# Optimization experiments

Hardware: AMD Instinct MI355X
Metric: run time of the kernel (lower is better)

The kernel has to match this reference:

```python
import jax, jax.numpy as jnp
import numpy as np

D_MODEL = 384
HEADS = 8
DIM_HEAD = D_MODEL // HEADS
IH = IW = 32
N = IH * IW
D_FF = 1536
EPS = 1e-5


def _relative_index():
    # replicates torch buffer construction (meshgrid 'ij')
    gy, gx = np.meshgrid(np.arange(IH), np.arange(IW), indexing='ij')
    coords = np.stack([gy, gx]).reshape(2, -1)              # [2, N]
    rel = coords[:, :, None] - coords[:, None, :]           # [2, N, N]
    rel[0] += IH - 1
    rel[1] += IW - 1
    rel[0] *= 2 * IW - 1
    return (rel[0] + rel[1]).reshape(-1)                    # [N*N] int


def setup_inputs() -> dict:
    key = jax.random.key(0)
    ks = jax.random.split(key, 16)
    s = 0.02
    return {
        'src': jax.random.normal(ks[0], (8, N, D_MODEL), jnp.float32),
        'pos': jax.random.normal(ks[1], (8, N, D_MODEL), jnp.float32),
        'rel_bias_table': jax.random.normal(ks[2], ((2 * IH - 1) * (2 * IW - 1), HEADS), jnp.float32) * s,
        'Wq': jax.random.normal(ks[3], (D_MODEL, D_MODEL), jnp.float32) * s,
        'Wk': jax.random.normal(ks[4], (D_MODEL, D_MODEL), jnp.float32) * s,
        'Wv': jax.random.normal(ks[5], (D_MODEL, D_MODEL), jnp.float32) * s,
        'Wo': jax.random.normal(ks[6], (D_MODEL, D_MODEL), jnp.float32) * s,
        'bo': jnp.zeros((D_MODEL,), jnp.float32),
        'W1': jax.random.normal(ks[7], (D_MODEL, D_FF), jnp.float32) * s,
        'b1': jnp.zeros((D_FF,), jnp.float32),
        'W2': jax.random.normal(ks[8], (D_FF, D_MODEL), jnp.float32) * s,
        'b2': jnp.zeros((D_MODEL,), jnp.float32),
        'g1': jnp.ones((D_MODEL,), jnp.float32),
        'be1': jnp.zeros((D_MODEL,), jnp.float32),
        'g2': jnp.ones((D_MODEL,), jnp.float32),
        'be2': jnp.zeros((D_MODEL,), jnp.float32),
    }


def _layernorm(x, g, b):
    mu = jnp.mean(x, -1, keepdims=True)
    var = jnp.var(x, -1, keepdims=True)
    return (x - mu) * jax.lax.rsqrt(var + EPS) * g + b


def _heads(x):
    b, n, _ = x.shape
    return x.reshape(b, n, HEADS, DIM_HEAD).transpose(0, 2, 1, 3)  # [b,h,n,d]


def reference(src, pos, rel_bias_table, Wq, Wk, Wv, Wo, bo, W1, b1, W2, b2, g1, be1, g2, be2):
    rel_idx = _relative_index()
    qk_in = src + pos
    q = _heads(qk_in @ Wq)
    k = _heads(qk_in @ Wk)
    v = _heads(src @ Wv)
    # relative bias: [heads, n, n]
    bias = rel_bias_table[rel_idx].reshape(N, N, HEADS).transpose(2, 0, 1)
    # relative_bias_x = (x^T @ bias)^T  ==  sum_m bias[h,m,n] * x[b,h,m,d]
    q = q + jnp.einsum('hmn,bhmd->bhnd', bias, q)
    k = k + jnp.einsum('hmn,bhmd->bhnd', bias, k)
    v = v + jnp.einsum('hmn,bhmd->bhnd', bias, v)
    scale = DIM_HEAD ** -0.5
    dots = jnp.einsum('bhnd,bhmd->bhnm', q, k) * scale
    attn = jax.nn.softmax(dots, axis=-1)
    out = jnp.einsum('bhnm,bhmd->bhnd', attn, v)
    out = out.transpose(0, 2, 1, 3).reshape(src.shape[0], N, D_MODEL)
    out = out @ Wo + bo
    x = _layernorm(src + out, g1, be1)
    ff = jax.nn.gelu(x @ W1 + b1, approximate=False) @ W2 + b2
    return _layernorm(x + ff, g2, be2)
```

## Files before the change

kernel.cpp:

```cpp
#include <hip/hip_runtime.h>
#include <math.h>

#define D_MODEL 384
#define HEADS 8
#define DIM_HEAD 48
#define NTOK 1024
#define BATCH 8
#define D_FF 1536
#define LN_EPS 1e-5f

typedef unsigned short u16;
typedef unsigned int u32;
typedef unsigned long long u64;
typedef short short8 __attribute__((ext_vector_type(8)));
typedef float f32x4 __attribute__((ext_vector_type(4)));

union F8 { short8 v; u64 q[2]; u16 u[8]; uint4 u4; };

__device__ __forceinline__ u16 f2bf(float f) {
    union { float f; unsigned u; } c; c.f = f;
    unsigned r = c.u + 0x7FFFu + ((c.u >> 16) & 1u);
    return (u16)(r >> 16);
}
__device__ __forceinline__ float bf2f(u16 u) {
    union { unsigned u; float f; } c; c.u = ((unsigned)u) << 16; return c.f;
}
__device__ __forceinline__ void gload_lds16(const u16* g, u16* l) {
    __builtin_amdgcn_global_load_lds(
        (const __attribute__((address_space(1))) void*)g,
        (__attribute__((address_space(3))) void*)l, 16, 0, 0);
}

__global__ __launch_bounds__(256) void add_cast_kernel(
        const float4* __restrict__ a, const float4* __restrict__ b,
        ushort4* __restrict__ o1, ushort4* __restrict__ o2, int n4) {
    int i = blockIdx.x * blockDim.x + threadIdx.x;
    if (i >= n4) return;
    float4 x = a[i], y = b[i];
    ushort4 u1, u2;
    u1.x = f2bf(x.x + y.x); u1.y = f2bf(x.y + y.y); u1.z = f2bf(x.z + y.z); u1.w = f2bf(x.w + y.w);
    u2.x = f2bf(x.x); u2.y = f2bf(x.y); u2.z = f2bf(x.z); u2.w = f2bf(x.w);
    o1[i] = u1; o2[i] = u2;
}

__global__ __launch_bounds__(256) void castT4_kernel(
        const float* __restrict__ i0, const float* __restrict__ i1,
        const float* __restrict__ i2, const float* __restrict__ i3,
        u16* __restrict__ o0, u16* __restrict__ o1,
        u16* __restrict__ o2, u16* __restrict__ o3) {
    const float* in  = (blockIdx.z == 0) ? i0 : (blockIdx.z == 1) ? i1 : (blockIdx.z == 2) ? i2 : i3;
    u16*         out = (blockIdx.z == 0) ? o0 : (blockIdx.z == 1) ? o1 : (blockIdx.z == 2) ? o2 : o3;
    __shared__ float t[32][33];
    int c0 = blockIdx.x * 32, r0 = blockIdx.y * 32;
    int tx = threadIdx.x, ty = threadIdx.y;
    for (int i = ty; i < 32; i += 8)
        t[i][tx] = in[(long)(r0 + i) * 384 + c0 + tx];
    __syncthreads();
    for (int i = ty; i < 32; i += 8)
        out[(long)(c0 + i) * 384 + r0 + tx] = f2bf(t[tx][i]);
}

__global__ __launch_bounds__(256) void castT_kernel(
        const float* __restrict__ in, u16* __restrict__ out, int R, int C) {
    __shared__ float t[32][33];
    int c0 = blockIdx.x * 32, r0 = blockIdx.y * 32;
    int tx = threadIdx.x, ty = threadIdx.y;
    for (int i = ty; i < 32; i += 8)
        t[i][tx] = in[(long)(r0 + i) * C + c0 + tx];
    __syncthreads();
    for (int i = ty; i < 32; i += 8)
        out[(long)(c0 + i) * R + r0 + tx] = f2bf(t[tx][i]);
}

__global__ __launch_bounds__(256) void biasT_bf16_kernel(const float* __restrict__ table,
                                                         u16* __restrict__ BT) {
    long i = (long)blockIdx.x * blockDim.x + threadIdx.x;
    const long total = (long)HEADS * NTOK * NTOK;
    if (i >= total) return;
    int m = (int)(i & 1023);
    int n = (int)((i >> 10) & 1023);
    int h = (int)(i >> 20);
    int dy = (m >> 5) - (n >> 5) + 31;
    int dx = (m & 31) - (n & 31) + 31;
    BT[i] = f2bf(table[(dy * 63 + dx) * HEADS + h]);
}

template<int OUTMODE, bool HAS_BIAS, bool HAS_RES, bool GELU_>
__global__ __launch_bounds__(256) void mgemm128_kernel(
        const u16* __restrict__ Ab, const u16* __restrict__ Btb,
        float* __restrict__ Cf, u16* __restrict__ Cb, u16* __restrict__ Ct,
        const float* __restrict__ bias, const float* __restrict__ Rb,
        int Kd, int lda, int ldbt, int ldc, int ldr) {
    __shared__ u16 As[2][128 * 32];
    __shared__ u16 Bs[2][128 * 32];
    int tid = threadIdx.x, wave = tid >> 6, lane = tid & 63, g = lane >> 4, l15 = lane & 15;
    int wm = wave >> 1, wn = wave & 1;
    int row0 = blockIdx.y * 128, col0 = blockIdx.x * 128;

    f32x4 acc[4][4] = {};

    int sr = lane >> 2, sk = lane & 3;
    const u16* aG0 = Ab  + (long)(row0 + wave * 16 + sr) * lda  + sk * 8;
    const u16* aG1 = Ab  + (long)(row0 + (wave + 4) * 16 + sr) * lda  + sk * 8;
    const u16* bG0 = Btb + (long)(col0 + wave * 16 + sr) * ldbt + sk * 8;
    const u16* bG1 = Btb + (long)(col0 + (wave + 4) * 16 + sr) * ldbt + sk * 8;
    int w0off = (wave * 16) * 32, w1off = ((wave + 4) * 16) * 32;

    const int T = Kd >> 5;
    gload_lds16(aG0, &As[0][w0off]);
    gload_lds16(aG1, &As[0][w1off]);
    gload_lds16(bG0, &Bs[0][w0off]);
    gload_lds16(bG1, &Bs[0][w1off]);
    __builtin_amdgcn_sched_barrier(0);

    for (int t = 0; t < T; ++t) {
        int cur = t & 1, nxt = cur ^ 1;
        if (t + 1 < T) {
            int k1 = (t + 1) << 5;
            gload_lds16(aG0 + k1, &As[nxt][w0off]);
            gload_lds16(aG1 + k1, &As[nxt][w1off]);
            gload_lds16(bG0 + k1, &Bs[nxt][w0off]);
            gload_lds16(bG1 + k1, &Bs[nxt][w1off]);
            __builtin_amdgcn_sched_barrier(0);
            asm volatile("s_waitcnt vmcnt(4)" ::: "memory");
        } else {
            asm volatile("s_waitcnt vmcnt(0)" ::: "memory");
        }
        __builtin_amdgcn_sched_barrier(0);
        __builtin_amdgcn_s_barrier();
        __builtin_amdgcn_sched_barrier(0);
        F8 af[4], bfr[4];
#pragma unroll
        for (int fm = 0; fm < 4; ++fm)
            af[fm].u4 = *(const uint4*)&As[cur][(wm * 64 + fm * 16 + l15) * 32 + g * 8];
#pragma unroll
        for (int fn = 0; fn < 4; ++fn)
            bfr[fn].u4 = *(const uint4*)&Bs[cur][(wn * 64 + fn * 16 + l15) * 32 + g * 8];
#pragma unroll
        for (int fm = 0; fm < 4; ++fm)
#pragma unroll
            for (int fn = 0; fn < 4; ++fn)
                acc[fm][fn] = __builtin_amdgcn_mfma_f32_16x16x32_bf16(
                    af[fm].v, bfr[fn].v, acc[fm][fn], 0, 0, 0);
        __builtin_amdgcn_sched_barrier(0);
        __builtin_amdgcn_s_barrier();
        __builtin_amdgcn_sched_barrier(0);
    }

#pragma unroll
    for (int fm = 0; fm < 4; ++fm) {
        int rbase = row0 + wm * 64 + fm * 16 + g * 4;
#pragma unroll
        for (int fn = 0; fn < 4; ++fn) {
            int c = col0 + wn * 64 + fn * 16 + l15;
            float bv = HAS_BIAS ? bias[c] : 0.f;
            float vs[4];
#pragma unroll
            for (int r = 0; r < 4; ++r) {
                float v = acc[fm][fn][r] + bv;
                if (HAS_RES) v += Rb[(long)(rbase + r) * ldr + c];
                if (GELU_)   v = 0.5f * v * (1.f + erff(v * 0.70710678118654752f));
                vs[r] = v;
                if (OUTMODE & 1) Cf[(long)(rbase + r) * ldc + c] = v;
                if (OUTMODE & 2) Cb[(long)(rbase + r) * ldc + c] = f2bf(v);
            }
            if (OUTMODE & 8) {
                int hh2 = (c * 683) >> 15; int dd = c - hh2 * 48;
                int bb2 = rbase >> 10;     int mm = rbase & 1023;
                ushort4 o;
                o.x = f2bf(vs[0]); o.y = f2bf(vs[1]); o.z = f2bf(vs[2]); o.w = f2bf(vs[3]);
                *(ushort4*)&Ct[(long)hh2 * 393216 + (long)(bb2 * 48 + dd) * 1024 + mm] = o;
            }
        }
    }
}

__global__ __launch_bounds__(256) void bias3_kernel(
        const u16* __restrict__ BT, const u16* __restrict__ QtH,
        const u16* __restrict__ KtH, const u16* __restrict__ VtH,
        u16* __restrict__ Q2H, u16* __restrict__ K2H, u16* __restrict__ V2T) {
    int bid = blockIdx.x;
    int widx = (bid & 7) * 96 + (bid >> 3);
    int h = widx / 96;
    int rem = widx - h * 96;
    int ry = rem / 6, cx = rem - ry * 6;
    const long hb = (long)h * 393216;
    const u16* A = BT + (long)h * 1048576;
    __shared__ u16 As[2][64 * 32];
    __shared__ u16 Bq[2][64 * 32], Bk[2][64 * 32], Bv[2][64 * 32];
    int tid = threadIdx.x, wave = tid >> 6, lane = tid & 63, g = lane >> 4, l15 = lane & 15;
    int wm = wave >> 1, wn = wave & 1;
    int row0 = ry * 64, col0 = cx * 64;
    f32x4 acc[3][2][2] = {};

    int sr = lane >> 2, sk = lane & 3;
    const u16* aG = A   + (long)(row0 + wave * 16 + sr) * 1024 + sk * 8;
    const u16* qG = QtH + hb + (long)(col0 + wave * 16 + sr) * 1024 + sk * 8;
    const u16* kG = KtH + hb + (long)(col0 + wave * 16 + sr) * 1024 + sk * 8;
    const u16* vG = VtH + hb + (long)(col0 + wave * 16 + sr) * 1024 + sk * 8;
    int woff = (wave * 16) * 32;

    gload_lds16(aG, &As[0][woff]);
    gload_lds16(qG, &Bq[0][woff]);
    gload_lds16(kG, &Bk[0][woff]);
    gload_lds16(vG, &Bv[0][woff]);
    __builtin_amdgcn_sched_barrier(0);

    for (int t = 0; t < 32; ++t) {
        int cur = t & 1, nxt = cur ^ 1;
        if (t + 1 < 32) {
            int k1 = (t + 1) << 5;
            gload_lds16(aG + k1, &As[nxt][woff]);
            gload_lds16(qG + k1, &Bq[nxt][woff]);
            gload_lds16(kG + k1, &Bk[nxt][woff]);
            gload_lds16(vG + k1, &Bv[nxt][woff]);
            __builtin_amdgcn_sched_barrier(0);
            asm volatile("s_waitcnt vmcnt(4)" ::: "memory");
        } else {
            asm volatile("s_waitcnt vmcnt(0)" ::: "memory");
        }
        __builtin_amdgcn_sched_barrier(0);
        __builtin_amdgcn_s_barrier();
        __builtin_amdgcn_sched_barrier(0);
        F8 af0, af1, b0, b1;
        af0.u4 = *(const uint4*)&As[cur][(wm * 32 + l15) * 32 + g * 8];
        af1.u4 = *(const uint4*)&As[cur][(wm * 32 + 16 + l15) * 32 + g * 8];
        b0.u4 = *(const uint4*)&Bq[cur][(wn * 32 + l15) * 32 + g * 8];
        b1.u4 = *(const uint4*)&Bq[cur][(wn * 32 + 16 + l15) * 32 + g * 8];
        acc[0][0][0] = __builtin_amdgcn_mfma_f32_16x16x32_bf16(af0.v, b0.v, acc[0][0][0], 0, 0, 0);
        acc[0][0][1] = __builtin_amdgcn_mfma_f32_16x16x32_bf16(af0.v, b1.v, acc[0][0][1], 0, 0, 0);
        acc[0][1][0] = __builtin_amdgcn_mfma_f32_16x16x32_bf16(af1.v, b0.v, acc[0][1][0], 0, 0, 0);
        acc[0][1][1] = __builtin_amdgcn_mfma_f32_16x16x32_bf16(af1.v, b1.v, acc[0][1][1], 0, 0, 0);
        b0.u4 = *(const uint4*)&Bk[cur][(wn * 32 + l15) * 32 + g * 8];
        b1.u4 = *(const uint4*)&Bk[cur][(wn * 32 + 16 + l15) * 32 + g * 8];
        acc[1][0][0] = __builtin_amdgcn_mfma_f32_16x16x32_bf16(af0.v, b0.v, acc[1][0][0], 0, 0, 0);
        acc[1][0][1] = __builtin_amdgcn_mfma_f32_16x16x32_bf16(af0.v, b1.v, acc[1][0][1], 0, 0, 0);
        acc[1][1][0] = __builtin_amdgcn_mfma_f32_16x16x32_bf16(af1.v, b0.v, acc[1][1][0], 0, 0, 0);
        acc[1][1][1] = __builtin_amdgcn_mfma_f32_16x16x32_bf16(af1.v, b1.v, acc[1][1][1], 0, 0, 0);
        b0.u4 = *(const uint4*)&Bv[cur][(wn * 32 + l15) * 32 + g * 8];
        b1.u4 = *(const uint4*)&Bv[cur][(wn * 32 + 16 + l15) * 32 + g * 8];
        acc[2][0][0] = __builtin_amdgcn_mfma_f32_16x16x32_bf16(af0.v, b0.v, acc[2][0][0], 0, 0, 0);
        acc[2][0][1] = __builtin_amdgcn_mfma_f32_16x16x32_bf16(af0.v, b1.v, acc[2][0][1], 0, 0, 0);
        acc[2][1][0] = __builtin_amdgcn_mfma_f32_16x16x32_bf16(af1.v, b0.v, acc[2][1][0], 0, 0, 0);
        acc[2][1][1] = __builtin_amdgcn_mfma_f32_16x16x32_bf16(af1.v, b1.v, acc[2][1][1], 0, 0, 0);
        __builtin_amdgcn_sched_barrier(0);
        __builtin_amdgcn_s_barrier();
        __builtin_amdgcn_sched_barrier(0);
    }

    const float qsc = 0.14433756729740643f * 1.4426950408889634f;
#pragma unroll
    for (int fm = 0; fm < 2; ++fm) {
        int rbase = row0 + wm * 32 + fm * 16 + g * 4;
#pragma unroll
        for (int fn = 0; fn < 2; ++fn) {
            int c = col0 + wn * 32 + fn * 16 + l15;
            int b2 = (c * 683) >> 15, d = c - b2 * 48;
            long bh = (long)h * 8 + b2;
            ushort4 rq = *(const ushort4*)&QtH[hb + (long)c * 1024 + rbase];
            ushort4 rk = *(const ushort4*)&KtH[hb + (long)c * 1024 + rbase];
            ushort4 rv = *(const ushort4*)&VtH[hb + (long)c * 1024 + rbase];
            const u16* rqa = (const u16*)&rq;
            const u16* rka = (const u16*)&rk;
            const u16* rva = (const u16*)&rv;
            int ks = d >> 5, g3 = (d >> 3) & 3, e = d & 7;
            long qbase = ((bh * 64 + (rbase >> 4)) * 8 + ks * 4 + g3) * 128
                       + (rbase & 15) * 8 + e;
            ushort4 vo;
            u16* voa = (u16*)&vo;
#pragma unroll
            for (int r = 0; r < 4; ++r) {
                float qv = acc[0][fm][fn][r] + bf2f(rqa[r]);
                Q2H[qbase + r * 8] = f2bf(qv * qsc);
                float kv = acc[1][fm][fn][r] + bf2f(rka[r]);
                K2H[qbase + r * 8] = f2bf(kv);
                voa[r] = f2bf(acc[2][fm][fn][r] + bf2f(rva[r]));
            }
            long vaddr = ((((bh * 16 + (rbase >> 6)) * 3 + (d >> 4)) * 2
                          + ((rbase >> 5) & 1)) * 4 + ((rbase >> 3) & 3)) * 128
                       + (d & 15) * 8 + (rbase & 7);
            *(ushort4*)&V2T[vaddr] = vo;
            if (d < 16) {
                long pbase = ((bh * 64 + (rbase >> 4)) * 8 + 4 + 2 + (d >> 3)) * 128
                           + (rbase & 15) * 8 + (d & 7);
#pragma unroll
                for (int r = 0; r < 4; ++r) {
                    Q2H[pbase + r * 8] = 0;
                    K2H[pbase + r * 8] = 0;
                }
            }
        }
    }
}

__global__ __launch_bounds__(256, 4) void attn_mfma_kernel(
        const u16* __restrict__ Q2H, const u16* __restrict__ K2H,
        const u16* __restrict__ V2T, u16* __restrict__ O) {
    int bid = blockIdx.x;
    int widx = (bid & 7) * 512 + (bid >> 3);
    int qb = widx & 63;
    int h  = (widx >> 6) & 7;
    int b  = widx >> 9;
    int tid = threadIdx.x, wave = tid >> 6, lane = tid & 63, g = lane >> 4, l15 = lane & 15;

    __shared__ char smem[13824];
    u16   (*Pl)[16][72]  = (u16(*)[16][72])smem;
    float (*Oc)[16][52]  = (float(*)[16][52])smem;
    float (*MLc)[16][2]  = (float(*)[16][2])(smem + 13312);
    const int sw = ((l15 >> 3) & 1) << 5;
    const int loff = (g * 16 + l15) * 8;

    const long bh = (long)(h * 8 + b);
    const u16* qtile = Q2H + (bh * 64 + qb) * 1024;
    F8 qf0, qf1;
    qf0.u4 = *(const uint4*)(qtile + loff);
    qf1.u4 = *(const uint4*)(qtile + 512 + loff);

    f32x4 oacc[3] = {};
    float runm = -1e30f, runl = 0.f;

#pragma unroll
    for (int it = 0; it < 4; ++it) {
        f32x4 s[4] = {};
#pragma unroll
        for (int mt = 0; mt < 4; ++mt) {
            const u16* ktile = K2H + (bh * 64 + wave * 16 + it * 4 + mt) * 1024;
            F8 kf0, kf1;
            kf0.u4 = *(const uint4*)(ktile + loff);
            kf1.u4 = *(const uint4*)(ktile + 512 + loff);
            s[mt] = __builtin_amdgcn_mfma_f32_16x16x32_bf16(kf0.v, qf0.v, s[mt], 0, 0, 0);
            s[mt] = __builtin_amdgcn_mfma_f32_16x16x32_bf16(kf1.v, qf1.v, s[mt], 0, 0, 0);
        }

        const u16* vtile = V2T + (bh * 16 + wave * 4 + it) * 3072;
        F8 vf[3][2];
#pragma unroll
        for (int dt = 0; dt < 3; ++dt)
#pragma unroll
            for (int ks = 0; ks < 2; ++ks)
                vf[dt][ks].u4 = *(const uint4*)(vtile + (dt * 2 + ks) * 512 + loff);

        float p[16];
#pragma unroll
        for (int i = 0; i < 16; ++i) p[i] = s[i >> 2][i & 3];
        float pm[8];
#pragma unroll
        for (int i = 0; i < 8; ++i) pm[i] = fmaxf(p[i], p[i + 8]);
#pragma unroll
        for (int st = 4; st > 0; st >>= 1)
#pragma unroll
            for (int i = 0; i < st; ++i) pm[i] = fmaxf(pm[i], pm[i + st]);
        float tmax = pm[0];
        tmax = fmaxf(tmax, __shfl_xor(tmax, 16));
        tmax = fmaxf(tmax, __shfl_xor(tmax, 32));
        if (!__all(tmax <= runm + 8.0f)) {
            float nm = fmaxf(runm, tmax);
            float corr = __builtin_amdgcn_exp2f(runm - nm);
            runm = nm; runl *= corr;
#pragma unroll
            for (int dt = 0; dt < 3; ++dt) {
                oacc[dt][0] *= corr; oacc[dt][1] *= corr;
                oacc[dt][2] *= corr; oacc[dt][3] *= corr;
            }
        }
        float ps = 0.f;
#pragma unroll
        for (int i = 0; i < 16; ++i) { p[i] = __builtin_amdgcn_exp2f(p[i] - runm); ps += p[i]; }
        ps += __shfl_xor(ps, 16);
        ps += __shfl_xor(ps, 32);
        runl += ps;

#pragma unroll
        for (int mt = 0; mt < 4; ++mt) {
            u32 wa, wb;
            asm("v_cvt_pk_bf16_f32 %0, %1, %2" : "=v"(wa) : "v"(p[mt * 4]), "v"(p[mt * 4 + 1]));
            asm("v_cvt_pk_bf16_f32 %0, %1, %2" : "=v"(wb) : "v"(p[mt * 4 + 2]), "v"(p[mt * 4 + 3]));
            *(u64*)&Pl[wave][l15][(mt * 16 + g * 4) ^ sw] = ((u64)wb << 32) | wa;
        }
        F8 pb[2];
#pragma unroll
        for (int ks = 0; ks < 2; ++ks) {
            pb[ks].q[0] = *(const u64*)&Pl[wave][l15][(ks * 32 + g * 8) ^ sw];
            pb[ks].q[1] = *(const u64*)&Pl[wave][l15][((ks * 32 + g * 8) + 4) ^ sw];
        }

#pragma unroll
        for (int dt = 0; dt < 3; ++dt) {
            oacc[dt] = __builtin_amdgcn_mfma_f32_16x16x32_bf16(vf[dt][0].v, pb[0].v, oacc[dt], 0, 0, 0);
            oacc[dt] = __builtin_amdgcn_mfma_f32_16x16x32_bf16(vf[dt][1].v, pb[1].v, oacc[dt], 0, 0, 0);
        }
    }

    __syncthreads();
#pragma unroll
    for (int dt = 0; dt < 3; ++dt)
#pragma unroll
        for (int r = 0; r < 4; ++r)
            Oc[wave][l15][dt * 16 + g * 4 + r] = oacc[dt][r];
    if (g == 0) { MLc[wave][l15][0] = runm; MLc[wave][l15][1] = runl; }
    __syncthreads();

    if (wave == 0) {
        float mm[4], cc[4];
#pragma unroll
        for (int w = 0; w < 4; ++w) mm[w] = MLc[w][l15][0];
        float M = fmaxf(fmaxf(mm[0], mm[1]), fmaxf(mm[2], mm[3]));
        float LL = 0.f;
#pragma unroll
        for (int w = 0; w < 4; ++w) {
            cc[w] = __builtin_amdgcn_exp2f(mm[w] - M);
            LL += cc[w] * MLc[w][l15][1];
        }
        float inv = 1.f / LL;
        u16* op = O + ((long)b * NTOK + qb * 16 + l15) * D_MODEL + h * DIM_HEAD;
#pragma unroll
        for (int dt = 0; dt < 3; ++dt) {
            ushort4 o;
#pragma unroll
            for (int r = 0; r < 4; ++r) {
                int d = dt * 16 + g * 4 + r;
                float v = cc[0] * Oc[0][l15][d] + cc[1] * Oc[1][l15][d]
                        + cc[2] * Oc[2][l15][d] + cc[3] * Oc[3][l15][d];
                ((u16*)&o)[r] = f2bf(v * inv);
            }
            *(ushort4*)(op + dt * 16 + g * 4) = o;
        }
    }
}

__global__ __launch_bounds__(128) void ln_kernel(
        const float* __restrict__ X, const float* __restrict__ Rb,
        const float* __restrict__ g, const float* __restrict__ be,
        float* __restrict__ O, u16* __restrict__ Obf, int hasRes) {
    int row = blockIdx.x;
    int tid = threadIdx.x;
    const float* x = X + (long)row * D_MODEL;
    float v[3];
#pragma unroll
    for (int l = 0; l < 3; ++l) {
        int c = tid + l * 128;
        v[l] = x[c];
        if (hasRes) v[l] += Rb[(long)row * D_MODEL + c];
    }
    __shared__ float red[128];
    float s = v[0] + v[1] + v[2];
    red[tid] = s; __syncthreads();
    for (int st = 64; st > 0; st >>= 1) {
        if (tid < st) red[tid] += red[tid + st];
        __syncthreads();
    }
    float mean = red[0] * (1.f / 384.f);
    __syncthreads();
    float sq = 0.f;
#pragma unroll
    for (int l = 0; l < 3; ++l) { float d = v[l] - mean; sq += d * d; }
    red[tid] = sq; __syncthreads();
    for (int st = 64; st > 0; st >>= 1) {
        if (tid < st) red[tid] += red[tid + st];
        __syncthreads();
    }
    float rstd = rsqrtf(red[0] * (1.f / 384.f) + LN_EPS);
#pragma unroll
    for (int l = 0; l < 3; ++l) {
        int c = tid + l * 128;
        float o = (v[l] - mean) * rstd * g[c] + be[c];
        O[(long)row * D_MODEL + c] = o;
        if (Obf) Obf[(long)row * D_MODEL + c] = f2bf(o);
    }
}

extern "C" void kernel_launch(void* const* d_in, const int* in_sizes, int n_in,
                              void* d_out, int out_size, void* d_ws, size_t ws_size,
                              hipStream_t stream) {
    const float* src   = (const float*)d_in[0];
    const float* pos   = (const float*)d_in[1];
    const float* table = (const float*)d_in[2];
    const float* Wq  = (const float*)d_in[3];
    const float* Wk  = (const float*)d_in[4];
    const float* Wv  = (const float*)d_in[5];
    const float* Wo  = (const float*)d_in[6];
    const float* bo  = (const float*)d_in[7];
    const float* W1  = (const float*)d_in[8];
    const float* b1  = (const float*)d_in[9];
    const float* W2  = (const float*)d_in[10];
    const float* b2  = (const float*)d_in[11];
    const float* g1  = (const float*)d_in[12];
    const float* be1 = (const float*)d_in[13];
    const float* g2  = (const float*)d_in[14];
    const float* be2 = (const float*)d_in[15];
    float* out = (float*)d_out;
    u16* ws = (u16*)d_ws;

    const long SZ = (long)BATCH * NTOK * D_MODEL;

    u16* WqT  = ws + 0;
    u16* WkT  = ws + 147456;
    u16* WvT  = ws + 294912;
    u16* WoT  = ws + 442368;
    u16* W1T  = ws + 589824;
    u16* W2T  = ws + 1179648;
    u16* QKin = ws + 1769472;
    u16* SRCB = ws + 4915200;
    u16* QtH  = ws + 8060928;
    u16* KtH  = ws + 11206656;
    u16* VtH  = ws + 14352384;
    u16* BT   = ws + 17498112;
    u16* ATT  = ws + 17498112;
    u16* Q2H  = ws + 25886720;
    u16* K2H  = ws + 30081024;
    u16* V2T  = ws + 34275328;
    float* Of  = (float*)(ws + 8060928);
    float* xf  = (float*)(ws + 14352384);
    u16*   xbf = QKin;
    u16*   hbf = Q2H;
    float* ff  = (float*)(ws + 8060928);

    add_cast_kernel<<<(int)(SZ / 4 + 255) / 256, 256, 0, stream>>>(
        (const float4*)src, (const float4*)pos, (ushort4*)QKin, (ushort4*)SRCB, (int)(SZ / 4));
    dim3 tb(32, 8);
    castT4_kernel<<<dim3(12, 12, 4), tb, 0, stream>>>(Wq, Wk, Wv, Wo, WqT, WkT, WvT, WoT);
    castT_kernel<<<dim3(48, 12), tb, 0, stream>>>(W1, W1T, 384, 1536);
    castT_kernel<<<dim3(12, 48), tb, 0, stream>>>(W2, W2T, 1536, 384);
    biasT_bf16_kernel<<<32768, 256, 0, stream>>>(table, BT);
    mgemm128_kernel<8, false, false, false><<<dim3(6, 64), 256, 0, stream>>>(
        QKin, WqT, nullptr, nullptr, QtH, nullptr, nullptr,
        384, 384, 384, 0, 0);
    mgemm128_kernel<8, false, false, false><<<dim3(3, 64), 256, 0, stream>>>(
        SRCB, WvT, nullptr, nullptr, VtH, nullptr, nullptr,
        384, 384, 384, 0, 0);
    bias3_kernel<<<768, 256, 0, stream>>>(BT, QtH, KtH, VtH, Q2H, K2H, V2T);
    attn_mfma_kernel<<<4096, 256, 0, stream>>>(Q2H, K2H, V2T, ATT);
    mgemm128_kernel<1, true, true, false><<<dim3(3, 64), 256, 0, stream>>>(
        ATT, WoT, Of, nullptr, nullptr, bo, src,
        384, 384, 384, 384, 384);
    ln_kernel<<<8192, 128, 0, stream>>>(Of, nullptr, g1, be1, xf, xbf, 0);
    mgemm128_kernel<2, true, false, true><<<dim3(12, 64), 256, 0, stream>>>(
        xbf, W1T, nullptr, hbf, nullptr, b1, nullptr,
        384, 384, 384, 1536, 0);
    mgemm128_kernel<1, true, true, false><<<dim3(3, 64), 256, 0, stream>>>(
        hbf, W2T, ff, nullptr, nullptr, b2, xf,
        1536, 1536, 1536, 384, 384);
    ln_kernel<<<8192, 128, 0, stream>>>(ff, nullptr, g2, be2, out, nullptr, 0);
}
```

Before: 229.0 us.

## Process two query tiles per attention block to reuse K/V fragment loads

Each attention workgroup now handles 32 query rows (two 16-row tiles) instead of 16, so every K and V fragment loaded from global memory feeds two sets of MFMAs and two online-softmax states. The grid is halved to match, and the min-blocks hint is dropped from launch bounds so the compiler can use more registers for the doubled accumulators. This is meant to cut K/V load traffic per unit of work, at the cost of higher register pressure, possibly lower occupancy, and a serialized two-pass cross-wave reduction at the end.

```diff
diff --git a/kernel.cpp b/kernel.cpp
--- a/kernel.cpp
+++ b/kernel.cpp
@@ -293,14 +293,14 @@
     }
 }
 
-__global__ __launch_bounds__(256, 4) void attn_mfma_kernel(
+__global__ __launch_bounds__(256) void attn_mfma_kernel(
         const u16* __restrict__ Q2H, const u16* __restrict__ K2H,
         const u16* __restrict__ V2T, u16* __restrict__ O) {
     int bid = blockIdx.x;
-    int widx = (bid & 7) * 512 + (bid >> 3);
-    int qb = widx & 63;
-    int h  = (widx >> 6) & 7;
-    int b  = widx >> 9;
+    int widx = (bid & 7) * 256 + (bid >> 3);
+    int qb = widx & 31;
+    int h  = (widx >> 5) & 7;
+    int b  = widx >> 8;
     int tid = threadIdx.x, wave = tid >> 6, lane = tid & 63, g = lane >> 4, l15 = lane & 15;
 
     __shared__ char smem[13824];
@@ -311,25 +311,29 @@
     const int loff = (g * 16 + l15) * 8;
 
     const long bh = (long)(h * 8 + b);
-    const u16* qtile = Q2H + (bh * 64 + qb) * 1024;
-    F8 qf0, qf1;
-    qf0.u4 = *(const uint4*)(qtile + loff);
-    qf1.u4 = *(const uint4*)(qtile + 512 + loff);
-
-    f32x4 oacc[3] = {};
-    float runm = -1e30f, runl = 0.f;
+    const u16* qt = Q2H + (bh * 64 + qb * 2) * 1024;
+    F8 qA0, qA1, qB0, qB1;
+    qA0.u4 = *(const uint4*)(qt + loff);
+    qA1.u4 = *(const uint4*)(qt + 512 + loff);
+    qB0.u4 = *(const uint4*)(qt + 1024 + loff);
+    qB1.u4 = *(const uint4*)(qt + 1536 + loff);
+
+    f32x4 oacc0[3] = {}, oacc1[3] = {};
+    float runm0 = -1e30f, runl0 = 0.f, runm1 = -1e30f, runl1 = 0.f;
 
 #pragma unroll
     for (int it = 0; it < 4; ++it) {
-        f32x4 s[4] = {};
+        f32x4 s0[4] = {}, s1[4] = {};
 #pragma unroll
         for (int mt = 0; mt < 4; ++mt) {
             const u16* ktile = K2H + (bh * 64 + wave * 16 + it * 4 + mt) * 1024;
             F8 kf0, kf1;
             kf0.u4 = *(const uint4*)(ktile + loff);
             kf1.u4 = *(const uint4*)(ktile + 512 + loff);
-            s[mt] = __builtin_amdgcn_mfma_f32_16x16x32_bf16(kf0.v, qf0.v, s[mt], 0, 0, 0);
-            s[mt] = __builtin_amdgcn_mfma_f32_16x16x32_bf16(kf1.v, qf1.v, s[mt], 0, 0, 0);
+            s0[mt] = __builtin_amdgcn_mfma_f32_16x16x32_bf16(kf0.v, qA0.v, s0[mt], 0, 0, 0);
+            s0[mt] = __builtin_amdgcn_mfma_f32_16x16x32_bf16(kf1.v, qA1.v, s0[mt], 0, 0, 0);
+            s1[mt] = __builtin_amdgcn_mfma_f32_16x16x32_bf16(kf0.v, qB0.v, s1[mt], 0, 0, 0);
+            s1[mt] = __builtin_amdgcn_mfma_f32_16x16x32_bf16(kf1.v, qB1.v, s1[mt], 0, 0, 0);
         }
 
         const u16* vtile = V2T + (bh * 16 + wave * 4 + it) * 3072;
@@ -340,90 +344,103 @@
             for (int ks = 0; ks < 2; ++ks)
                 vf[dt][ks].u4 = *(const uint4*)(vtile + (dt * 2 + ks) * 512 + loff);
 
-        float p[16];
-#pragma unroll
-        for (int i = 0; i < 16; ++i) p[i] = s[i >> 2][i & 3];
-        float pm[8];
-#pragma unroll
-        for (int i = 0; i < 8; ++i) pm[i] = fmaxf(p[i], p[i + 8]);
-#pragma unroll
-        for (int st = 4; st > 0; st >>= 1)
-#pragma unroll
-            for (int i = 0; i < st; ++i) pm[i] = fmaxf(pm[i], pm[i + st]);
-        float tmax = pm[0];
-        tmax = fmaxf(tmax, __shfl_xor(tmax, 16));
-        tmax = fmaxf(tmax, __shfl_xor(tmax, 32));
-        if (!__all(tmax <= runm + 8.0f)) {
-            float nm = fmaxf(runm, tmax);
-            float corr = __builtin_amdgcn_exp2f(runm - nm);
-            runm = nm; runl *= corr;
+#pragma unroll
+        for (int qi = 0; qi < 2; ++qi) {
+            f32x4* s = qi ? s1 : s0;
+            float& runm = qi ? runm1 : runm0;
+            float& runl = qi ? runl1 : runl0;
+            f32x4* oacc = qi ? oacc1 : oacc0;
+
+            float p[16];
+#pragma unroll
+            for (int i = 0; i < 16; ++i) p[i] = s[i >> 2][i & 3];
+            float pm[8];
+#pragma unroll
+            for (int i = 0; i < 8; ++i) pm[i] = fmaxf(p[i], p[i + 8]);
+#pragma unroll
+            for (int st = 4; st > 0; st >>= 1)
+#pragma unroll
+                for (int i = 0; i < st; ++i) pm[i] = fmaxf(pm[i], pm[i + st]);
+            float tmax = pm[0];
+            tmax = fmaxf(tmax, __shfl_xor(tmax, 16));
+            tmax = fmaxf(tmax, __shfl_xor(tmax, 32));
+            if (!__all(tmax <= runm + 8.0f)) {
+                float nm = fmaxf(runm, tmax);
+                float corr = __builtin_amdgcn_exp2f(runm - nm);
+                runm = nm; runl *= corr;
+#pragma unroll
+                for (int dt = 0; dt < 3; ++dt) {
+                    oacc[dt][0] *= corr; oacc[dt][1] *= corr;
+                    oacc[dt][2] *= corr; oacc[dt][3] *= corr;
+                }
+            }
+            float ps = 0.f;
+#pragma unroll
+            for (int i = 0; i < 16; ++i) { p[i] = __builtin_amdgcn_exp2f(p[i] - runm); ps += p[i]; }
+            ps += __shfl_xor(ps, 16);
+            ps += __shfl_xor(ps, 32);
+            runl += ps;
+
+#pragma unroll
+            for (int mt = 0; mt < 4; ++mt) {
+                u32 wa, wb;
+                asm("v_cvt_pk_bf16_f32 %0, %1, %2" : "=v"(wa) : "v"(p[mt * 4]), "v"(p[mt * 4 + 1]));
+                asm("v_cvt_pk_bf16_f32 %0, %1, %2" : "=v"(wb) : "v"(p[mt * 4 + 2]), "v"(p[mt * 4 + 3]));
+                *(u64*)&Pl[wave][l15][(mt * 16 + g * 4) ^ sw] = ((u64)wb << 32) | wa;
+            }
+            F8 pb[2];
+#pragma unroll
+            for (int ks = 0; ks < 2; ++ks) {
+                pb[ks].q[0] = *(const u64*)&Pl[wave][l15][(ks * 32 + g * 8) ^ sw];
+                pb[ks].q[1] = *(const u64*)&Pl[wave][l15][((ks * 32 + g * 8) + 4) ^ sw];
+            }
 #pragma unroll
             for (int dt = 0; dt < 3; ++dt) {
-                oacc[dt][0] *= corr; oacc[dt][1] *= corr;
-                oacc[dt][2] *= corr; oacc[dt][3] *= corr;
-            }
-        }
-        float ps = 0.f;
-#pragma unroll
-        for (int i = 0; i < 16; ++i) { p[i] = __builtin_amdgcn_exp2f(p[i] - runm); ps += p[i]; }
-        ps += __shfl_xor(ps, 16);
-        ps += __shfl_xor(ps, 32);
-        runl += ps;
-
-#pragma unroll
-        for (int mt = 0; mt < 4; ++mt) {
-            u32 wa, wb;
-            asm("v_cvt_pk_bf16_f32 %0, %1, %2" : "=v"(wa) : "v"(p[mt * 4]), "v"(p[mt * 4 + 1]));
-            asm("v_cvt_pk_bf16_f32 %0, %1, %2" : "=v"(wb) : "v"(p[mt * 4 + 2]), "v"(p[mt * 4 + 3]));
-            *(u64*)&Pl[wave][l15][(mt * 16 + g * 4) ^ sw] = ((u64)wb << 32) | wa;
-        }
-        F8 pb[2];
-#pragma unroll
-        for (int ks = 0; ks < 2; ++ks) {
-            pb[ks].q[0] = *(const u64*)&Pl[wave][l15][(ks * 32 + g * 8) ^ sw];
-            pb[ks].q[1] = *(const u64*)&Pl[wave][l15][((ks * 32 + g * 8) + 4) ^ sw];
-        }
-
-#pragma unroll
-        for (int dt = 0; dt < 3; ++dt) {
-            oacc[dt] = __builtin_amdgcn_mfma_f32_16x16x32_bf16(vf[dt][0].v, pb[0].v, oacc[dt], 0, 0, 0);
-            oacc[dt] = __builtin_amdgcn_mfma_f32_16x16x32_bf16(vf[dt][1].v, pb[1].v, oacc[dt], 0, 0, 0);
-        }
-    }
-
-    __syncthreads();
-#pragma unroll
-    for (int dt = 0; dt < 3; ++dt)
-#pragma unroll
-        for (int r = 0; r < 4; ++r)
-            Oc[wave][l15][dt * 16 + g * 4 + r] = oacc[dt][r];
-    if (g == 0) { MLc[wave][l15][0] = runm; MLc[wave][l15][1] = runl; }
-    __syncthreads();
-
-    if (wave == 0) {
-        float mm[4], cc[4];
-#pragma unroll
-        for (int w = 0; w < 4; ++w) mm[w] = MLc[w][l15][0];
-        float M = fmaxf(fmaxf(mm[0], mm[1]), fmaxf(mm[2], mm[3]));
-        float LL = 0.f;
-#pragma unroll
-        for (int w = 0; w < 4; ++w) {
-            cc[w] = __builtin_amdgcn_exp2f(mm[w] - M);
-            LL += cc[w] * MLc[w][l15][1];
-        }
-        float inv = 1.f / LL;
-        u16* op = O + ((long)b * NTOK + qb * 16 + l15) * D_MODEL + h * DIM_HEAD;
-#pragma unroll
-        for (int dt = 0; dt < 3; ++dt) {
-            ushort4 o;
-#pragma unroll
-            for (int r = 0; r < 4; ++r) {
-                int d = dt * 16 + g * 4 + r;
-                float v = cc[0] * Oc[0][l15][d] + cc[1] * Oc[1][l15][d]
-                        + cc[2] * Oc[2][l15][d] + cc[3] * Oc[3][l15][d];
-                ((u16*)&o)[r] = f2bf(v * inv);
-            }
-            *(ushort4*)(op + dt * 16 + g * 4) = o;
+                oacc[dt] = __builtin_amdgcn_mfma_f32_16x16x32_bf16(vf[dt][0].v, pb[0].v, oacc[dt], 0, 0, 0);
+                oacc[dt] = __builtin_amdgcn_mfma_f32_16x16x32_bf16(vf[dt][1].v, pb[1].v, oacc[dt], 0, 0, 0);
+            }
+        }
+    }
+
+#pragma unroll
+    for (int qi = 0; qi < 2; ++qi) {
+        f32x4* oacc = qi ? oacc1 : oacc0;
+        float runm = qi ? runm1 : runm0;
+        float runl = qi ? runl1 : runl0;
+        __syncthreads();
+#pragma unroll
+        for (int dt = 0; dt < 3; ++dt)
+#pragma unroll
+            for (int r = 0; r < 4; ++r)
+                Oc[wave][l15][dt * 16 + g * 4 + r] = oacc[dt][r];
+        if (g == 0) { MLc[wave][l15][0] = runm; MLc[wave][l15][1] = runl; }
+        __syncthreads();
+
+        if (wave == 0) {
+            float mm[4], cc[4];
+#pragma unroll
+            for (int w = 0; w < 4; ++w) mm[w] = MLc[w][l15][0];
+            float M = fmaxf(fmaxf(mm[0], mm[1]), fmaxf(mm[2], mm[3]));
+            float LL = 0.f;
+#pragma unroll
+            for (int w = 0; w < 4; ++w) {
+                cc[w] = __builtin_amdgcn_exp2f(mm[w] - M);
+                LL += cc[w] * MLc[w][l15][1];
+            }
+            float inv = 1.f / LL;
+            u16* op = O + ((long)b * NTOK + qb * 32 + qi * 16 + l15) * D_MODEL + h * DIM_HEAD;
+#pragma unroll
+            for (int dt = 0; dt < 3; ++dt) {
+                ushort4 o;
+#pragma unroll
+                for (int r = 0; r < 4; ++r) {
+                    int d = dt * 16 + g * 4 + r;
+                    float v = cc[0] * Oc[0][l15][d] + cc[1] * Oc[1][l15][d]
+                            + cc[2] * Oc[2][l15][d] + cc[3] * Oc[3][l15][d];
+                    ((u16*)&o)[r] = f2bf(v * inv);
+                }
+                *(ushort4*)(op + dt * 16 + g * 4) = o;
+            }
         }
     }
 }
@@ -529,7 +546,7 @@
         SRCB, WvT, nullptr, nullptr, VtH, nullptr, nullptr,
         384, 384, 384, 0, 0);
     bias3_kernel<<<768, 256, 0, stream>>>(BT, QtH, KtH, VtH, Q2H, K2H, V2T);
-    attn_mfma_kernel<<<4096, 256, 0, stream>>>(Q2H, K2H, V2T, ATT);
+    attn_mfma_kernel<<<2048, 256, 0, stream>>>(Q2H, K2H, V2T, ATT);
     mgemm128_kernel<1, true, true, false><<<dim3(3, 64), 256, 0, stream>>>(
         ATT, WoT, Of, nullptr, nullptr, bo, src,
         384, 384, 384, 384, 384);
```

Measured after the change: 227.4 us. Within noise of the previous version (-0.7%).
